# Kernel tuning notes

Measured on AMD Instinct MI355X. Metric: run time of the kernel, lower is better.

Reference implementation:

```python
import jax, jax.numpy as jnp
import numpy as np

B, T, D_MODEL, H, D = 2, 2048, 2048, 16, 128


def _rope_tables(t, d_half, base=10000.0):
    inv_freq = 1.0 / (base ** (jnp.arange(d_half, dtype=jnp.float32) / d_half))
    ang = jnp.arange(t, dtype=jnp.float32)[:, None] * inv_freq[None, :]  # (T, D/2)
    return jnp.cos(ang), jnp.sin(ang)


def setup_inputs() -> dict:
    key = jax.random.key(0)
    ks = jax.random.split(key, 5)
    x = jax.random.normal(ks[0], (B, T, D_MODEL), dtype=jnp.float32)
    mask = jnp.tril(jnp.ones((T, T), dtype=bool))  # causal boolean mask
    cos, sin = _rope_tables(T, D // 2)
    std = 1.0 / np.sqrt(D_MODEL)
    Wq = jax.random.normal(ks[1], (D_MODEL, H * D), dtype=jnp.float32) * std
    Wk = jax.random.normal(ks[2], (D_MODEL, H * D), dtype=jnp.float32) * std
    Wv = jax.random.normal(ks[3], (D_MODEL, H * D), dtype=jnp.float32) * std
    Wo = jax.random.normal(ks[4], (H * D, D_MODEL), dtype=jnp.float32) * std
    return {"x": x, "mask": mask, "cos": cos, "sin": sin,
            "Wq": Wq, "Wk": Wk, "Wv": Wv, "Wo": Wo}


def _apply_rope(x, cos, sin):
    # x: (B, H, T, D); cos/sin: (T, D/2)
    half = x.shape[-1] // 2
    x1, x2 = x[..., :half], x[..., half:]
    c = cos[None, None]
    s = sin[None, None]
    return jnp.concatenate([x1 * c - x2 * s, x1 * s + x2 * c], axis=-1)


def reference(x, mask, cos, sin, Wq, Wk, Wv, Wo):
    b, t, _ = x.shape
    scale = 1.0 / np.sqrt(D)
    # projections: (B, T, H*D) -> (B, H, T, D)
    q = (x @ Wq).reshape(b, t, H, D).transpose(0, 2, 1, 3)
    k = (x @ Wk).reshape(b, t, H, D).transpose(0, 2, 1, 3)
    v = (x @ Wv).reshape(b, t, H, D).transpose(0, 2, 1, 3)
    q = _apply_rope(q, cos, sin)
    k = _apply_rope(k, cos, sin)
    scores = jnp.einsum('bhqd,bhkd->bhqk', q, k) * scale
    scores = jnp.where(mask[None, None], scores, jnp.float32(-1e30))
    attn = jax.nn.softmax(scores, axis=-1)
    out = jnp.einsum('bhqk,bhkd->bhqd', attn, v)  # (B, H, T, D)
    out = out.transpose(0, 2, 1, 3).reshape(b, t, H * D)
    return out @ Wo
```

## Files before the change

kernel.cpp:

```cpp
#include <hip/hip_runtime.h>

#define T_SEQ 2048
#define DM    2048
#define NH    16
#define HD    128
#define NROW  4096

typedef __attribute__((ext_vector_type(8))) short short8;
typedef __attribute__((ext_vector_type(4))) float f32x4;
typedef __attribute__((ext_vector_type(16))) float f32x16;

static __device__ __forceinline__ float bf2f(unsigned short h) {
    unsigned int u = ((unsigned int)h) << 16;
    return __builtin_bit_cast(float, u);
}
static __device__ __forceinline__ unsigned short f2bf(float f) {
    unsigned int u = __builtin_bit_cast(unsigned int, f);
    u += 0x7FFFu + ((u >> 16) & 1u);
    return (unsigned short)(u >> 16);
}
static __device__ __forceinline__ unsigned short bf_fast(float f) {
    return (unsigned short)((__builtin_bit_cast(unsigned int, f) + 0x8000u) >> 16);
}

typedef __attribute__((address_space(1))) const unsigned int gas_uint;
typedef __attribute__((address_space(3))) unsigned int las_uint;

static __device__ __forceinline__ void load_lds16(const void* g, void* l) {
    __builtin_amdgcn_global_load_lds((gas_uint*)g, (las_uint*)l, 16, 0, 0);
}

static __device__ __forceinline__ f32x4 mfma_bf16(short8 a, short8 b, f32x4 c) {
    return __builtin_amdgcn_mfma_f32_16x16x32_bf16(a, b, c, 0, 0, 0);
}
static __device__ __forceinline__ f32x16 mfma32_bf16(short8 a, short8 b, f32x16 c) {
    return __builtin_amdgcn_mfma_f32_32x32x16_bf16(a, b, c, 0, 0, 0);
}

__global__ __launch_bounds__(256) void k_cast(const float* __restrict__ x,
                                              unsigned short* __restrict__ xb, int n) {
    int idx = (blockIdx.x * 256 + threadIdx.x) * 4;
    if (idx >= n) return;
    float4 v = *(const float4*)(x + idx);
    ushort4 o;
    o.x = f2bf(v.x); o.y = f2bf(v.y); o.z = f2bf(v.z); o.w = f2bf(v.w);
    *(ushort4*)(xb + idx) = o;
}

__global__ __launch_bounds__(256) void k_transpose(const float* __restrict__ w0, const float* __restrict__ w1,
                                                   const float* __restrict__ w2, const float* __restrict__ w3,
                                                   unsigned short* __restrict__ t0, unsigned short* __restrict__ t1,
                                                   unsigned short* __restrict__ t2, unsigned short* __restrict__ t3) {
    __shared__ float tile[32][33];
    int z = blockIdx.z;
    const float* W = (z == 0) ? w0 : (z == 1) ? w1 : (z == 2) ? w2 : w3;
    unsigned short* Wt = (z == 0) ? t0 : (z == 1) ? t1 : (z == 2) ? t2 : t3;
    int bx = blockIdx.x * 32;
    int by = blockIdx.y * 32;
    int tx = threadIdx.x, ty = threadIdx.y;
#pragma unroll
    for (int i = 0; i < 4; ++i)
        tile[ty + i * 8][tx] = W[(size_t)(by + ty + i * 8) * DM + bx + tx];
    __syncthreads();
#pragma unroll
    for (int i = 0; i < 4; ++i)
        Wt[(size_t)(bx + ty + i * 8) * DM + by + tx] = f2bf(tile[tx][ty + i * 8]);
}

template <bool FOUT>
static __device__ __forceinline__ void gemm_body(const unsigned short* __restrict__ A,
                                                 const unsigned short* __restrict__ Bt,
                                                 unsigned short* __restrict__ Cb,
                                                 float* __restrict__ Cf) {
    __shared__ unsigned short As[128 * 64];
    __shared__ unsigned short Bs[128 * 64];
    const int tid = threadIdx.x;
    const int w = tid >> 6, lane = tid & 63;
    const int col = lane & 15, quad = lane >> 4;
    const int wm = w >> 1, wn = w & 1;
    const size_t m0 = (size_t)blockIdx.y * 128;
    const size_t n0 = (size_t)blockIdx.x * 128;

    f32x4 acc[4][4];
#pragma unroll
    for (int i = 0; i < 4; ++i)
#pragma unroll
        for (int j = 0; j < 4; ++j)
            acc[i][j] = (f32x4){0.f, 0.f, 0.f, 0.f};

    const int lrow = lane >> 3;
    const int gcol = ((lane & 7) ^ lrow) * 8;

    for (int k0 = 0; k0 < DM; k0 += 64) {
#pragma unroll
        for (int c = w; c < 16; c += 4) {
            load_lds16(A + (m0 + c * 8 + lrow) * DM + k0 + gcol, &As[c * 512]);
            load_lds16(Bt + (n0 + c * 8 + lrow) * DM + k0 + gcol, &Bs[c * 512]);
        }
        __syncthreads();
#pragma unroll
        for (int ks = 0; ks < 2; ++ks) {
            short8 af[4], bf[4];
            int g = ks * 4 + quad;
#pragma unroll
            for (int mt = 0; mt < 4; ++mt) {
                int r = wm * 64 + mt * 16 + col;
                af[mt] = *(const short8*)&As[r * 64 + ((g ^ (r & 7)) * 8)];
            }
#pragma unroll
            for (int nt = 0; nt < 4; ++nt) {
                int r = wn * 64 + nt * 16 + col;
                bf[nt] = *(const short8*)&Bs[r * 64 + ((g ^ (r & 7)) * 8)];
            }
#pragma unroll
            for (int mt = 0; mt < 4; ++mt)
#pragma unroll
                for (int nt = 0; nt < 4; ++nt)
                    acc[mt][nt] = mfma_bf16(af[mt], bf[nt], acc[mt][nt]);
        }
        __syncthreads();
    }
#pragma unroll
    for (int mt = 0; mt < 4; ++mt)
#pragma unroll
        for (int nt = 0; nt < 4; ++nt)
#pragma unroll
            for (int reg = 0; reg < 4; ++reg) {
                size_t r = m0 + wm * 64 + mt * 16 + quad * 4 + reg;
                size_t c = n0 + wn * 64 + nt * 16 + col;
                if (FOUT) Cf[r * DM + c] = acc[mt][nt][reg];
                else      Cb[r * DM + c] = f2bf(acc[mt][nt][reg]);
            }
}

__global__ __launch_bounds__(256) void k_gemm_qkv(const unsigned short* __restrict__ xb,
                                                  const unsigned short* __restrict__ wtq,
                                                  const unsigned short* __restrict__ wtk,
                                                  const unsigned short* __restrict__ wtv,
                                                  unsigned short* __restrict__ qb,
                                                  unsigned short* __restrict__ kb,
                                                  unsigned short* __restrict__ vb) {
    int z = blockIdx.z;
    const unsigned short* Bt = (z == 0) ? wtq : (z == 1) ? wtk : wtv;
    unsigned short* C = (z == 0) ? qb : (z == 1) ? kb : vb;
    gemm_body<false>(xb, Bt, C, nullptr);
}

__global__ __launch_bounds__(256) void k_gemm_out(const unsigned short* __restrict__ ob,
                                                  const unsigned short* __restrict__ wto,
                                                  float* __restrict__ out) {
    gemm_body<true>(ob, wto, nullptr, out);
}

__global__ __launch_bounds__(256) void k_rope_k(unsigned short* __restrict__ K,
                                                const float* __restrict__ cosp,
                                                const float* __restrict__ sinp) {
    int idx = blockIdx.x * 256 + threadIdx.x;
    int d4 = (idx & 15) * 4;
    int h = (idx >> 4) & 15;
    int row = idx >> 8;
    int t = row & (T_SEQ - 1);
    size_t base = (size_t)row * DM + h * HD + d4;
    ushort4 x1 = *(const ushort4*)(K + base);
    ushort4 x2 = *(const ushort4*)(K + base + 64);
    float4 c = *(const float4*)(cosp + t * 64 + d4);
    float4 s = *(const float4*)(sinp + t * 64 + d4);
    ushort4 o1, o2;
#pragma unroll
    for (int i = 0; i < 4; ++i) {
        float a1 = bf2f(((const unsigned short*)&x1)[i]);
        float a2 = bf2f(((const unsigned short*)&x2)[i]);
        float cc = ((const float*)&c)[i], ss = ((const float*)&s)[i];
        ((unsigned short*)&o1)[i] = f2bf(a1 * cc - a2 * ss);
        ((unsigned short*)&o2)[i] = f2bf(a1 * ss + a2 * cc);
    }
    *(ushort4*)(K + base) = o1;
    *(ushort4*)(K + base + 64) = o2;
}

__global__ __launch_bounds__(256) void k_vtr(const unsigned short* __restrict__ V,
                                             unsigned short* __restrict__ Vt) {
    __shared__ unsigned short tile[64][68];
    int t0 = blockIdx.x * 64;
    int hd0 = blockIdx.y * 64;
    int b = blockIdx.z;
    int tid = threadIdx.x;
    int rr = tid >> 4, cc = (tid & 15) * 4;
#pragma unroll
    for (int it = 0; it < 4; ++it) {
        int row = it * 16 + rr;
        *(ushort4*)&tile[row][cc] =
            *(const ushort4*)(V + (size_t)(b * T_SEQ + t0 + row) * DM + hd0 + cc);
    }
    __syncthreads();
    int h = hd0 >> 7, d0 = hd0 & 127;
    size_t obase = (size_t)(b * NH + h) * HD;
#pragma unroll
    for (int it = 0; it < 4; ++it) {
        int lhd = it * 16 + rr;
        ushort4 v;
#pragma unroll
        for (int j = 0; j < 4; ++j) ((unsigned short*)&v)[j] = tile[cc + j][lhd];
        *(ushort4*)(Vt + (obase + d0 + lhd) * (size_t)T_SEQ + t0 + cc) = v;
    }
}

#define PST 72
__global__ __launch_bounds__(256) void k_flash(const unsigned short* __restrict__ Q,
                                               const unsigned short* __restrict__ K,
                                               const unsigned short* __restrict__ Vt,
                                               unsigned short* __restrict__ O,
                                               const float* __restrict__ cosp,
                                               const float* __restrict__ sinp) {
    __shared__ unsigned short Ks[64 * 128];
    __shared__ unsigned short Vs[128 * 64];
    __shared__ unsigned short Ps[4][32 * PST];
    const int tid = threadIdx.x;
    const int w = tid >> 6, lane = tid & 63;
    const int col = lane & 31, l5 = lane >> 5;
    const int flat = blockIdx.x | (blockIdx.y << 4) | (blockIdx.z << 8);
    const int j = 15 - (flat >> 5);
    const int hb = flat & 31;
    const int h = hb & 15, b = hb >> 4;
    const int q0 = j * 128;
    const size_t rowbase = ((size_t)b * T_SEQ) * DM + (size_t)h * HD;
    const size_t hbase = ((size_t)b * NH + h) * HD;
    const float SCL = 0.088388347648318447f * 1.4426950408889634f;
    unsigned short* Pw = &Ps[w][0];

    const int t = q0 + w * 32 + col;
    short8 qf[8];
    {
        const unsigned short* qp = Q + rowbase + (size_t)t * DM + l5 * 8;
#pragma unroll
        for (int st = 0; st < 8; ++st)
            qf[st] = *(const short8*)(qp + st * 16);
        const float* cp = cosp + t * 64 + l5 * 8;
        const float* sp = sinp + t * 64 + l5 * 8;
#pragma unroll
        for (int st = 0; st < 4; ++st) {
            float4 c0 = *(const float4*)(cp + st * 16);
            float4 c1 = *(const float4*)(cp + st * 16 + 4);
            float4 s0v = *(const float4*)(sp + st * 16);
            float4 s1v = *(const float4*)(sp + st * 16 + 4);
#pragma unroll
            for (int jj = 0; jj < 8; ++jj) {
                float cv = ((jj < 4) ? ((const float*)&c0)[jj] : ((const float*)&c1)[jj - 4]) * SCL;
                float sv = ((jj < 4) ? ((const float*)&s0v)[jj] : ((const float*)&s1v)[jj - 4]) * SCL;
                float a1 = bf2f((unsigned short)qf[st][jj]);
                float a2 = bf2f((unsigned short)qf[st + 4][jj]);
                qf[st][jj]     = (short)f2bf(a1 * cv - a2 * sv);
                qf[st + 4][jj] = (short)f2bf(a1 * sv + a2 * cv);
            }
        }
    }

    f32x16 o[4];
#pragma unroll
    for (int i = 0; i < 4; ++i) o[i] = (f32x16)(0.f);
    float m_i = -1e30f, l_i = 0.f;

    const int kt_max = 2 * j + 1;
    const int kt_lim = (q0 + w * 32 + 31) >> 6;
    const int cswz = col & 7;

    for (int kt = 0; kt <= kt_max; ++kt) {
        const int k0 = kt * 64;
        __syncthreads();
#pragma unroll
        for (int c = 0; c < 4; ++c) {
            const int c4 = w * 4 + c;
            const int krow = c4 * 4 + (lane >> 4);
            const int kpos = lane & 15;
            load_lds16(K + rowbase + (size_t)(k0 + krow) * DM + ((kpos ^ (krow & 7)) * 8),
                       &Ks[c4 * 512]);
            const int vrow = c4 * 8 + (lane >> 3);
            const int vpos = lane & 7;
            load_lds16(Vt + (hbase + vrow) * (size_t)T_SEQ + k0 + ((vpos ^ (vrow & 7)) * 8),
                       &Vs[c4 * 512]);
        }
        __syncthreads();
        if (kt > kt_lim) continue;

        f32x16 s0 = (f32x16)(0.f), s1 = (f32x16)(0.f);
#pragma unroll
        for (int st = 0; st < 8; ++st) {
            const int dg = (2 * st + l5) ^ cswz;
            short8 kf0 = *(const short8*)&Ks[col * 128 + dg * 8];
            short8 kf1 = *(const short8*)&Ks[col * 128 + 4096 + dg * 8];
            s0 = mfma32_bf16(kf0, qf[st], s0);
            s1 = mfma32_bf16(kf1, qf[st], s1);
        }

        if (k0 + 63 > q0 + w * 32) {
            const int kb = k0 + 4 * l5;
#pragma unroll
            for (int r = 0; r < 16; ++r) {
                const int key = kb + (r & 3) + 8 * (r >> 2);
                if (key > t) s0[r] = -1e30f;
                if (key + 32 > t) s1[r] = -1e30f;
            }
        }

        float mx = -1e30f;
#pragma unroll
        for (int r = 0; r < 16; ++r) mx = fmaxf(mx, fmaxf(s0[r], s1[r]));
        mx = fmaxf(mx, __shfl_xor(mx, 32));
        const float mnew = fmaxf(m_i, mx);
        const float alpha = __builtin_amdgcn_exp2f(m_i - mnew);
        m_i = mnew;
        float sum = 0.f;
#pragma unroll
        for (int r = 0; r < 16; ++r) {
            float p0 = __builtin_amdgcn_exp2f(s0[r] - mnew);
            float p1 = __builtin_amdgcn_exp2f(s1[r] - mnew);
            s0[r] = p0; s1[r] = p1;
            sum += p0 + p1;
        }
        sum += __shfl_xor(sum, 32);
        l_i = l_i * alpha + sum;
#pragma unroll
        for (int i = 0; i < 4; ++i) o[i] *= alpha;

#pragma unroll
        for (int g = 0; g < 4; ++g) {
            ushort4 a4, b4;
#pragma unroll
            for (int i = 0; i < 4; ++i) {
                ((unsigned short*)&a4)[i] = bf_fast(s0[g * 4 + i]);
                ((unsigned short*)&b4)[i] = bf_fast(s1[g * 4 + i]);
            }
            *(ushort4*)(Pw + col * PST + g * 8 + 4 * l5)      = a4;
            *(ushort4*)(Pw + col * PST + 32 + g * 8 + 4 * l5) = b4;
        }
        short8 pb[4];
#pragma unroll
        for (int st = 0; st < 4; ++st)
            pb[st] = *(const short8*)(Pw + col * PST + st * 16 + l5 * 8);

#pragma unroll
        for (int ms = 0; ms < 4; ++ms) {
            const int drow = (ms * 32 + col) * 64;
#pragma unroll
            for (int st = 0; st < 4; ++st) {
                const int kg = (2 * st + l5) ^ cswz;
                short8 vf = *(const short8*)&Vs[drow + kg * 8];
                o[ms] = mfma32_bf16(vf, pb[st], o[ms]);
            }
        }
    }

    const float inv = __builtin_amdgcn_rcpf(l_i);
    unsigned short* op = O + rowbase + (size_t)t * DM;
#pragma unroll
    for (int ms = 0; ms < 4; ++ms)
#pragma unroll
        for (int g = 0; g < 4; ++g) {
            ushort4 st4;
#pragma unroll
            for (int i = 0; i < 4; ++i)
                ((unsigned short*)&st4)[i] = bf_fast(o[ms][g * 4 + i] * inv);
            *(ushort4*)(op + ms * 32 + g * 8 + 4 * l5) = st4;
        }
}

extern "C" void kernel_launch(void* const* d_in, const int* in_sizes, int n_in,
                              void* d_out, int out_size, void* d_ws, size_t ws_size,
                              hipStream_t stream) {
    const float* x    = (const float*)d_in[0];
    const float* cosp = (const float*)d_in[2];
    const float* sinp = (const float*)d_in[3];
    const float* Wq   = (const float*)d_in[4];
    const float* Wk   = (const float*)d_in[5];
    const float* Wv   = (const float*)d_in[6];
    const float* Wo   = (const float*)d_in[7];
    float* out = (float*)d_out;

    unsigned short* xb  = (unsigned short*)d_ws;
    unsigned short* wtq = xb  + (size_t)NROW * DM;
    unsigned short* wtk = wtq + (size_t)DM * DM;
    unsigned short* wtv = wtk + (size_t)DM * DM;
    unsigned short* wto = wtv + (size_t)DM * DM;
    unsigned short* qb  = wto + (size_t)DM * DM;
    unsigned short* kb  = qb  + (size_t)NROW * DM;
    unsigned short* vb  = kb  + (size_t)NROW * DM;
    unsigned short* ob  = vb  + (size_t)NROW * DM;
    unsigned short* vt  = xb;

    hipLaunchKernelGGL(k_cast, dim3(8192), dim3(256), 0, stream, x, xb, NROW * DM);
    hipLaunchKernelGGL(k_transpose, dim3(64, 64, 4), dim3(32, 8), 0, stream,
                       Wq, Wk, Wv, Wo, wtq, wtk, wtv, wto);
    hipLaunchKernelGGL(k_gemm_qkv, dim3(16, 32, 3), dim3(256), 0, stream,
                       xb, wtq, wtk, wtv, qb, kb, vb);
    hipLaunchKernelGGL(k_rope_k, dim3(4096), dim3(256), 0, stream, kb, cosp, sinp);
    hipLaunchKernelGGL(k_vtr, dim3(32, 32, 2), dim3(256), 0, stream, vb, vt);
    hipLaunchKernelGGL(k_flash, dim3(16, 16, 2), dim3(256), 0, stream,
                       qb, kb, vt, ob, cosp, sinp);
    hipLaunchKernelGGL(k_gemm_out, dim3(16, 32, 1), dim3(256), 0, stream, ob, wto, out);
}
```

Before: 407.3 us.

## Rewrite projection GEMMs as double-buffered 256x128 tiles with 512 threads

Replaces the single-buffered 128x128 GEMM body with a 256x128 tile run by 8 waves, holding double-buffered LDS for A and B. Global-to-LDS loads for the next K slice are spread across the MFMA phases using explicit waitcnt, barriers and setprio. A flattened grid with an XCD-style block swizzle replaces the 3D grid. The aim is to hide global load latency and raise reuse per tile. In exchange it uses more LDS per block, adds many barriers, and relies on fragile hand-placed waitcnt values.

Measured after the change: 444.3 us. 9.1% more time.

```diff
diff --git a/kernel.cpp b/kernel.cpp
--- a/kernel.cpp
+++ b/kernel.cpp
@@ -68,18 +68,18 @@
 }
 
 template <bool FOUT>
-static __device__ __forceinline__ void gemm_body(const unsigned short* __restrict__ A,
-                                                 const unsigned short* __restrict__ Bt,
-                                                 unsigned short* __restrict__ Cb,
-                                                 float* __restrict__ Cf) {
-    __shared__ unsigned short As[128 * 64];
-    __shared__ unsigned short Bs[128 * 64];
+static __device__ __forceinline__ void gemm256_body(const unsigned short* __restrict__ A,
+                                                    const unsigned short* __restrict__ Bt,
+                                                    unsigned short* __restrict__ Cb,
+                                                    float* __restrict__ Cf,
+                                                    int m0, int n0) {
+    __shared__ unsigned short Asm_[2][256 * 64];
+    __shared__ unsigned short Bsm_[2][128 * 64];
     const int tid = threadIdx.x;
     const int w = tid >> 6, lane = tid & 63;
     const int col = lane & 15, quad = lane >> 4;
     const int wm = w >> 1, wn = w & 1;
-    const size_t m0 = (size_t)blockIdx.y * 128;
-    const size_t n0 = (size_t)blockIdx.x * 128;
+    const int csw = col & 7;
 
     f32x4 acc[4][4];
 #pragma unroll
@@ -88,68 +88,133 @@
         for (int j = 0; j < 4; ++j)
             acc[i][j] = (f32x4){0.f, 0.f, 0.f, 0.f};
 
-    const int lrow = lane >> 3;
-    const int gcol = ((lane & 7) ^ lrow) * 8;
-
-    for (int k0 = 0; k0 < DM; k0 += 64) {
-#pragma unroll
-        for (int c = w; c < 16; c += 4) {
-            load_lds16(A + (m0 + c * 8 + lrow) * DM + k0 + gcol, &As[c * 512]);
-            load_lds16(Bt + (n0 + c * 8 + lrow) * DM + k0 + gcol, &Bs[c * 512]);
-        }
-        __syncthreads();
-#pragma unroll
-        for (int ks = 0; ks < 2; ++ks) {
-            short8 af[4], bf[4];
-            int g = ks * 4 + quad;
-#pragma unroll
-            for (int mt = 0; mt < 4; ++mt) {
-                int r = wm * 64 + mt * 16 + col;
-                af[mt] = *(const short8*)&As[r * 64 + ((g ^ (r & 7)) * 8)];
-            }
-#pragma unroll
-            for (int nt = 0; nt < 4; ++nt) {
-                int r = wn * 64 + nt * 16 + col;
-                bf[nt] = *(const short8*)&Bs[r * 64 + ((g ^ (r & 7)) * 8)];
-            }
-#pragma unroll
-            for (int mt = 0; mt < 4; ++mt)
-#pragma unroll
-                for (int nt = 0; nt < 4; ++nt)
-                    acc[mt][nt] = mfma_bf16(af[mt], bf[nt], acc[mt][nt]);
-        }
-        __syncthreads();
-    }
+    const int srow = tid >> 3, sg = tid & 7;
+    const unsigned short* Ab = A  + (size_t)(m0 + srow) * DM + ((sg ^ (srow & 7)) * 8);
+    const unsigned short* Bb = Bt + (size_t)(n0 + srow) * DM + ((sg ^ (srow & 7)) * 8);
+
+#define STG_A(bf_, rb_, k_) load_lds16(Ab + (size_t)((rb_) * 64) * DM + (k_), \
+                                       &Asm_[bf_][(rb_) * 4096 + w * 512])
+#define STG_B(bf_, rb_, k_) load_lds16(Bb + (size_t)((rb_) * 64) * DM + (k_), \
+                                       &Bsm_[bf_][(rb_) * 4096 + w * 512])
+
+    STG_A(0, 0, 0); STG_A(0, 1, 0); STG_A(0, 2, 0); STG_A(0, 3, 0);
+    STG_B(0, 0, 0); STG_B(0, 1, 0);
+
+    short8 af[2][2];
+    short8 bfr[2][2][2];
+
+#define LDA(qm_) do {                                                                   \
+    const int rA0 = wm * 64 + ((qm_) * 2 + 0) * 16 + col;                               \
+    const int rA1 = wm * 64 + ((qm_) * 2 + 1) * 16 + col;                               \
+    af[0][0] = *(const short8*)&As[rA0 * 64 + (((0 + quad) ^ csw) * 8)];                \
+    af[0][1] = *(const short8*)&As[rA0 * 64 + (((4 + quad) ^ csw) * 8)];                \
+    af[1][0] = *(const short8*)&As[rA1 * 64 + (((0 + quad) ^ csw) * 8)];                \
+    af[1][1] = *(const short8*)&As[rA1 * 64 + (((4 + quad) ^ csw) * 8)];                \
+} while (0)
+
+#define LDB(qn_) do {                                                                   \
+    const int rB0 = wn * 64 + ((qn_) * 2 + 0) * 16 + col;                               \
+    const int rB1 = wn * 64 + ((qn_) * 2 + 1) * 16 + col;                               \
+    bfr[qn_][0][0] = *(const short8*)&Bs[rB0 * 64 + (((0 + quad) ^ csw) * 8)];          \
+    bfr[qn_][0][1] = *(const short8*)&Bs[rB0 * 64 + (((4 + quad) ^ csw) * 8)];          \
+    bfr[qn_][1][0] = *(const short8*)&Bs[rB1 * 64 + (((0 + quad) ^ csw) * 8)];          \
+    bfr[qn_][1][1] = *(const short8*)&Bs[rB1 * 64 + (((4 + quad) ^ csw) * 8)];          \
+} while (0)
+
+#define MM(qm_, qn_) do {                                                                             \
+    __builtin_amdgcn_s_setprio(1);                                                                    \
+    acc[(qm_)*2+0][(qn_)*2+0] = mfma_bf16(af[0][0], bfr[qn_][0][0], acc[(qm_)*2+0][(qn_)*2+0]);       \
+    acc[(qm_)*2+0][(qn_)*2+1] = mfma_bf16(af[0][0], bfr[qn_][1][0], acc[(qm_)*2+0][(qn_)*2+1]);       \
+    acc[(qm_)*2+1][(qn_)*2+0] = mfma_bf16(af[1][0], bfr[qn_][0][0], acc[(qm_)*2+1][(qn_)*2+0]);       \
+    acc[(qm_)*2+1][(qn_)*2+1] = mfma_bf16(af[1][0], bfr[qn_][1][0], acc[(qm_)*2+1][(qn_)*2+1]);       \
+    acc[(qm_)*2+0][(qn_)*2+0] = mfma_bf16(af[0][1], bfr[qn_][0][1], acc[(qm_)*2+0][(qn_)*2+0]);       \
+    acc[(qm_)*2+0][(qn_)*2+1] = mfma_bf16(af[0][1], bfr[qn_][1][1], acc[(qm_)*2+0][(qn_)*2+1]);       \
+    acc[(qm_)*2+1][(qn_)*2+0] = mfma_bf16(af[1][1], bfr[qn_][0][1], acc[(qm_)*2+1][(qn_)*2+0]);       \
+    acc[(qm_)*2+1][(qn_)*2+1] = mfma_bf16(af[1][1], bfr[qn_][1][1], acc[(qm_)*2+1][(qn_)*2+1]);       \
+    __builtin_amdgcn_s_setprio(0);                                                                    \
+} while (0)
+
+    const int NT = DM / 64;
+    for (int t = 0; t < NT; ++t) {
+        const int buf = t & 1, nbuf = buf ^ 1;
+        const int k1 = (t + 1) * 64;
+        const bool pf = (t + 1 < NT);
+        if (pf) { STG_A(nbuf, 0, k1); STG_A(nbuf, 1, k1); STG_B(nbuf, 0, k1); }
+        if (pf) asm volatile("s_waitcnt vmcnt(3)" ::: "memory");
+        else    asm volatile("s_waitcnt vmcnt(0)" ::: "memory");
+        __builtin_amdgcn_s_barrier();
+        __builtin_amdgcn_sched_barrier(0);
+
+        const unsigned short* As = Asm_[buf];
+        const unsigned short* Bs = Bsm_[buf];
+
+        LDA(0); LDB(0);
+        if (pf) { STG_A(nbuf, 2, k1); STG_A(nbuf, 3, k1); }
+        __builtin_amdgcn_s_barrier();
+        asm volatile("s_waitcnt lgkmcnt(0)" ::: "memory");
+        __builtin_amdgcn_sched_barrier(0);
+        MM(0, 0);
+        __builtin_amdgcn_s_barrier();
+
+        LDB(1);
+        if (pf) { STG_B(nbuf, 1, k1); }
+        __builtin_amdgcn_s_barrier();
+        asm volatile("s_waitcnt lgkmcnt(0)" ::: "memory");
+        __builtin_amdgcn_sched_barrier(0);
+        MM(0, 1);
+        __builtin_amdgcn_s_barrier();
+
+        LDA(1);
+        __builtin_amdgcn_s_barrier();
+        asm volatile("s_waitcnt lgkmcnt(0)" ::: "memory");
+        __builtin_amdgcn_sched_barrier(0);
+        MM(1, 1);
+        MM(1, 0);
+        __builtin_amdgcn_s_barrier();
+    }
+
+#undef STG_A
+#undef STG_B
+#undef LDA
+#undef LDB
+#undef MM
+
 #pragma unroll
     for (int mt = 0; mt < 4; ++mt)
 #pragma unroll
         for (int nt = 0; nt < 4; ++nt)
 #pragma unroll
             for (int reg = 0; reg < 4; ++reg) {
-                size_t r = m0 + wm * 64 + mt * 16 + quad * 4 + reg;
-                size_t c = n0 + wn * 64 + nt * 16 + col;
+                size_t r = (size_t)m0 + wm * 64 + mt * 16 + quad * 4 + reg;
+                size_t c = (size_t)n0 + wn * 64 + nt * 16 + col;
                 if (FOUT) Cf[r * DM + c] = acc[mt][nt][reg];
                 else      Cb[r * DM + c] = f2bf(acc[mt][nt][reg]);
             }
 }
 
-__global__ __launch_bounds__(256) void k_gemm_qkv(const unsigned short* __restrict__ xb,
-                                                  const unsigned short* __restrict__ wtq,
-                                                  const unsigned short* __restrict__ wtk,
-                                                  const unsigned short* __restrict__ wtv,
-                                                  unsigned short* __restrict__ qb,
-                                                  unsigned short* __restrict__ kb,
-                                                  unsigned short* __restrict__ vb) {
-    int z = blockIdx.z;
-    const unsigned short* Bt = (z == 0) ? wtq : (z == 1) ? wtk : wtv;
-    unsigned short* C = (z == 0) ? qb : (z == 1) ? kb : vb;
-    gemm_body<false>(xb, Bt, C, nullptr);
-}
-
-__global__ __launch_bounds__(256) void k_gemm_out(const unsigned short* __restrict__ ob,
-                                                  const unsigned short* __restrict__ wto,
-                                                  float* __restrict__ out) {
-    gemm_body<true>(ob, wto, nullptr, out);
+__global__ __launch_bounds__(512, 2) void k_gemm_qkv(const unsigned short* __restrict__ xb,
+                                                     const unsigned short* __restrict__ wtq,
+                                                     const unsigned short* __restrict__ wtk,
+                                                     const unsigned short* __restrict__ wtv,
+                                                     unsigned short* __restrict__ qb,
+                                                     unsigned short* __restrict__ kb,
+                                                     unsigned short* __restrict__ vb) {
+    const int flat = blockIdx.x;
+    const int swz = (flat & 7) * 96 + (flat >> 3);
+    const int tz = swz >> 8, rem = swz & 255;
+    const int tx = rem & 15, ty = rem >> 4;
+    const unsigned short* Bt = (tz == 0) ? wtq : (tz == 1) ? wtk : wtv;
+    unsigned short* C = (tz == 0) ? qb : (tz == 1) ? kb : vb;
+    gemm256_body<false>(xb, Bt, C, nullptr, ty * 256, tx * 128);
+}
+
+__global__ __launch_bounds__(512, 2) void k_gemm_out(const unsigned short* __restrict__ ob,
+                                                     const unsigned short* __restrict__ wto,
+                                                     float* __restrict__ out) {
+    const int flat = blockIdx.x;
+    const int swz = (flat & 7) * 32 + (flat >> 3);
+    const int tx = swz & 15, ty = swz >> 4;
+    gemm256_body<true>(ob, wto, nullptr, out, ty * 256, tx * 128);
 }
 
 __global__ __launch_bounds__(256) void k_rope_k(unsigned short* __restrict__ K,
@@ -390,11 +455,11 @@
     hipLaunchKernelGGL(k_cast, dim3(8192), dim3(256), 0, stream, x, xb, NROW * DM);
     hipLaunchKernelGGL(k_transpose, dim3(64, 64, 4), dim3(32, 8), 0, stream,
                        Wq, Wk, Wv, Wo, wtq, wtk, wtv, wto);
-    hipLaunchKernelGGL(k_gemm_qkv, dim3(16, 32, 3), dim3(256), 0, stream,
+    hipLaunchKernelGGL(k_gemm_qkv, dim3(768), dim3(512), 0, stream,
                        xb, wtq, wtk, wtv, qb, kb, vb);
     hipLaunchKernelGGL(k_rope_k, dim3(4096), dim3(256), 0, stream, kb, cosp, sinp);
     hipLaunchKernelGGL(k_vtr, dim3(32, 32, 2), dim3(256), 0, stream, vb, vt);
     hipLaunchKernelGGL(k_flash, dim3(16, 16, 2), dim3(256), 0, stream,
                        qb, kb, vt, ob, cosp, sinp);
-    hipLaunchKernelGGL(k_gemm_out, dim3(16, 32, 1), dim3(256), 0, stream, ob, wto, out);
-}
+    hipLaunchKernelGGL(k_gemm_out, dim3(256), dim3(512), 0, stream, ob, wto, out);
+}
```
